# Kernel optimization log

Measured on AMD Instinct MI355X. Metric: run time of the kernel, lower is better.

The kernel has to match this reference:

```python
import jax, jax.numpy as jnp
import numpy as np

N = 100000        # nodes
E = 1600000       # edges (avg degree 16)
F_IN = 64         # num_node_features
NHID = 64         # args.nhid
NCLS = 16         # num_classes
K1 = 8            # Chebyshev order of conv1


def setup_inputs() -> dict:
    key = jax.random.key(0)
    k0, k1, k2, k3 = jax.random.split(key, 4)
    x = jax.random.normal(k0, (N, F_IN), dtype=jnp.float32)
    edge_index = jax.random.randint(k1, (2, E), 0, N, dtype=jnp.int32)
    # ChebConv params: K linear maps (no per-lin bias) + one shared bias
    W1 = jax.random.normal(k2, (K1, F_IN, NHID), dtype=jnp.float32) * (1.0 / np.sqrt(F_IN))
    b1 = jnp.zeros((NHID,), dtype=jnp.float32)
    W2 = jax.random.normal(k3, (1, NHID, NCLS), dtype=jnp.float32) * (1.0 / np.sqrt(NHID))
    b2 = jnp.zeros((NCLS,), dtype=jnp.float32)
    return {"x": x, "edge_index": edge_index, "W1": W1, "b1": b1, "W2": W2, "b2": b2}


def _cheb_norm(edge_index, num_nodes):
    # PyG ChebConv.__norm__ with normalization='sym', lambda_max=2.0, unit edge weights:
    # remove self loops; L_hat = 2L/lambda_max - I = -D^{-1/2} A D^{-1/2}, diag = 0.
    row, col = edge_index[0], edge_index[1]
    nonself = (row != col).astype(jnp.float32)
    deg = jax.ops.segment_sum(nonself, row, num_segments=num_nodes)
    dinv = jnp.where(deg > 0, jax.lax.rsqrt(jnp.maximum(deg, 1.0)), 0.0)
    norm = -dinv[row] * dinv[col] * nonself
    return row, col, norm


def reference(x, edge_index, W1, b1, W2, b2):
    row, col, norm = _cheb_norm(edge_index, N)

    def prop(h):  # L_hat @ h via gather + scatter-add, [N,F]
        return jax.ops.segment_sum(h[col] * norm[:, None], row, num_segments=N)

    # conv1: ChebConv K=8 recursion  Tx_k = 2*L_hat*Tx_{k-1} - Tx_{k-2}
    tx_prev = x
    out = x @ W1[0]
    tx = prop(x)
    out = out + tx @ W1[1]
    for k in range(2, K1):
        tx_new = 2.0 * prop(tx) - tx_prev
        out = out + tx_new @ W1[k]
        tx_prev, tx = tx, tx_new
    h = jax.nn.relu(out + b1)
    # dropout: identity (eval mode)
    # conv2: ChebConv K=1 -> just Tx_0 = h
    logits = h @ W2[0] + b2
    return jax.nn.softmax(logits, axis=1)
```

## Files before the change

### kernel.cpp

```cpp
#include <hip/hip_runtime.h>
#include <hip/hip_fp16.h>

#define N_NODES 100000
#define N_EDGES 1600000
#define F 64
#define NCLS 16
#define K1 8
#define BSH 9
#define NBK 196
#define BROWS 512
#define BKCAP 9216
#define EPB 4096
#define COLBITS 17

using f16x8 = __attribute__((ext_vector_type(8))) _Float16;
using f32x4 = __attribute__((ext_vector_type(4))) float;

__global__ __launch_bounds__(256) void k_bucketA(const int* __restrict__ ei,
                                                 int* __restrict__ gcur,
                                                 unsigned* __restrict__ bk) {
    __shared__ int cnt[4][256];
    __shared__ int wbase[4][256];
    int tid = threadIdx.x;
    int w = tid >> 6;
    for (int i = tid; i < 1024; i += 256) ((int*)cnt)[i] = 0;
    __syncthreads();
    unsigned pe[16];
    int packed[16];
    int e0 = blockIdx.x * EPB;
#pragma unroll
    for (int u = 0; u < 16; u++) {
        int e = e0 + u * 256 + tid;
        packed[u] = -1;
        if (e < N_EDGES) {
            int r = ei[e], c = ei[N_EDGES + e];
            if (r != c) {
                int b = r >> BSH;
                pe[u] = ((unsigned)(r & (BROWS - 1)) << COLBITS) | (unsigned)c;
                int rank = atomicAdd(&cnt[w][b], 1);
                packed[u] = (rank << 8) | b;
            }
        }
    }
    __syncthreads();
    {
        int c0 = cnt[0][tid], c1 = cnt[1][tid], c2 = cnt[2][tid], c3 = cnt[3][tid];
        int tot = c0 + c1 + c2 + c3;
        int g = tot ? atomicAdd(&gcur[tid], tot) : 0;
        wbase[0][tid] = g;
        wbase[1][tid] = g + c0;
        wbase[2][tid] = g + c0 + c1;
        wbase[3][tid] = g + c0 + c1 + c2;
    }
    __syncthreads();
#pragma unroll
    for (int u = 0; u < 16; u++) {
        if (packed[u] >= 0) {
            int b = packed[u] & 255;
            int rank = packed[u] >> 8;
            bk[(size_t)b * BKCAP + wbase[w][b] + rank] = pe[u];
        }
    }
}

__global__ __launch_bounds__(256) void k_csrB(const unsigned* __restrict__ bk,
                                              const int* __restrict__ gcur,
                                              int* __restrict__ deg,
                                              float* __restrict__ dinv,
                                              int* __restrict__ rowptr,
                                              int* __restrict__ csr_col) {
    __shared__ int hist[BROWS];
    __shared__ int cur[BROWS];
    __shared__ int sd[256];
    __shared__ int sorted[BKCAP];
    int b = blockIdx.x;
    int tid = threadIdx.x;
    for (int i = tid; i < BROWS; i += 256) { hist[i] = 0; cur[i] = 0; }
    __syncthreads();
    int cnt = gcur[b];
    const unsigned* src = bk + (size_t)b * BKCAP;
    for (int i = tid; i < cnt; i += 256)
        atomicAdd(&hist[src[i] >> COLBITS], 1);
    __syncthreads();
    int v0 = hist[2 * tid], v1 = hist[2 * tid + 1];
    int s = v0 + v1;
    sd[tid] = s;
    __syncthreads();
    for (int d = 1; d < 256; d <<= 1) {
        int t = (tid >= d) ? sd[tid - d] : 0;
        __syncthreads();
        sd[tid] += t;
        __syncthreads();
    }
    int excl = sd[tid] - s;
    int rbase = b << BSH;
    int cbase = b * BKCAP;
    int gr0 = rbase + 2 * tid;
    int gr1 = gr0 + 1;
    if (gr0 < N_NODES) {
        deg[gr0] = v0;
        dinv[gr0] = v0 > 0 ? rsqrtf((float)v0) : 0.f;
        rowptr[gr0] = cbase + excl;
    }
    if (gr1 < N_NODES) {
        deg[gr1] = v1;
        dinv[gr1] = v1 > 0 ? rsqrtf((float)v1) : 0.f;
        rowptr[gr1] = cbase + excl + v0;
    }
    __syncthreads();
    hist[2 * tid] = excl;
    hist[2 * tid + 1] = excl + v0;
    __syncthreads();
    for (int i = tid; i < cnt; i += 256) {
        unsigned e = src[i];
        int rl = e >> COLBITS;
        int pos = hist[rl] + atomicAdd(&cur[rl], 1);
        sorted[pos] = (int)(e & ((1u << COLBITS) - 1));
    }
    __syncthreads();
    for (int i = tid; i < cnt; i += 256)
        csr_col[cbase + i] = sorted[i];
}

__global__ void k_cvt(const float* __restrict__ x, __half* __restrict__ t0) {
    int i = blockIdx.x * blockDim.x + threadIdx.x;
    int base = i * 4;
    if (base >= N_NODES * F) return;
    float4 v = *(const float4*)&x[base];
    __half2 a = __floats2half2_rn(v.x, v.y);
    __half2 b = __floats2half2_rn(v.z, v.w);
    *(__half2*)&t0[base] = a;
    *(__half2*)&t0[base + 2] = b;
}

__global__ void k_prepW(const float* __restrict__ W1, __half* __restrict__ Wf) {
    int t = blockIdx.x * blockDim.x + threadIdx.x;
    if (t >= K1 * 2 * 4 * 64) return;
    int lane = t & 63;
    int cb = (t >> 6) & 3;
    int fg = (t >> 8) & 1;
    int kidx = t >> 9;
    int col = cb * 16 + (lane & 15);
    int kbase = fg * 32 + (lane >> 4) * 8;
    f16x8 v;
#pragma unroll
    for (int j = 0; j < 8; j++)
        v[j] = (_Float16)W1[kidx * 4096 + (kbase + j) * 64 + col];
    *(f16x8*)(Wf + (size_t)t * 8) = v;
}

__global__ __launch_bounds__(256) void k_prop(const int* __restrict__ rowptr,
                                              const int* __restrict__ deg,
                                              const int* __restrict__ csr_col,
                                              const float* __restrict__ dinv,
                                              const __half* __restrict__ src,
                                              const __half* __restrict__ prev,
                                              __half* __restrict__ dst,
                                              float alpha, float beta) {
    int wpair = (int)((blockIdx.x * blockDim.x + threadIdx.x) >> 6);
    int lane = threadIdx.x & 63;
    int nA = wpair * 2;
    if (nA >= N_NODES) return;
    int h = lane >> 5;
    int hl = lane & 31;
    int s3 = (lane >> 3) & 3;
    int fb = (lane & 7) * 8;
    int node = nA + h;
    bool valid = node < N_NODES;
    int cb  = valid ? rowptr[node] : 0;
    int end = valid ? cb + deg[node] : 0;
    float dn = valid ? dinv[node] : 0.f;

    float acc[8] = {};

    while (true) {
        int n_own = end - cb;
        if (n_own > 32) n_own = 32;
        if (n_own < 0) n_own = 0;
        int n_oth = __shfl(n_own, lane ^ 32, 64);
        int nmax = n_own > n_oth ? n_own : n_oth;
        if (nmax == 0) break;
        int col = 0;
        float dv = 0.f;
        if (hl < n_own) {
            col = csr_col[cb + hl];
            dv = dinv[col];
        }
        for (int j = 0; j < nmax; j += 16) {
            int cc[4];
            float ww[4];
#pragma unroll
            for (int g = 0; g < 4; g++) {
                int sl = (h << 5) | (j + g * 4 + s3);
                cc[g] = __shfl(col, sl, 64);
                ww[g] = __shfl(dv, sl, 64);
            }
            uint4 raw[4];
#pragma unroll
            for (int g = 0; g < 4; g++)
                raw[g] = *(const uint4*)(src + (size_t)cc[g] * F + fb);
#pragma unroll
            for (int g = 0; g < 4; g++) {
                float2 f0 = __half22float2(*(__half2*)&raw[g].x);
                float2 f1 = __half22float2(*(__half2*)&raw[g].y);
                float2 f2 = __half22float2(*(__half2*)&raw[g].z);
                float2 f3 = __half22float2(*(__half2*)&raw[g].w);
                acc[0] = fmaf(ww[g], f0.x, acc[0]);
                acc[1] = fmaf(ww[g], f0.y, acc[1]);
                acc[2] = fmaf(ww[g], f1.x, acc[2]);
                acc[3] = fmaf(ww[g], f1.y, acc[3]);
                acc[4] = fmaf(ww[g], f2.x, acc[4]);
                acc[5] = fmaf(ww[g], f2.y, acc[5]);
                acc[6] = fmaf(ww[g], f3.x, acc[6]);
                acc[7] = fmaf(ww[g], f3.y, acc[7]);
            }
        }
        cb += n_own;
    }

#pragma unroll
    for (int i = 0; i < 8; i++) {
        acc[i] += __shfl_xor(acc[i], 8, 64);
        acc[i] += __shfl_xor(acc[i], 16, 64);
    }

    if ((lane & 24) == 0 && valid) {
        float scale = -alpha * dn;
        float r[8];
#pragma unroll
        for (int i = 0; i < 8; i++) r[i] = scale * acc[i];
        if (beta != 0.f) {
            uint4 pv = *(const uint4*)(prev + (size_t)node * F + fb);
            float2 p0 = __half22float2(*(__half2*)&pv.x);
            float2 p1 = __half22float2(*(__half2*)&pv.y);
            float2 p2 = __half22float2(*(__half2*)&pv.z);
            float2 p3 = __half22float2(*(__half2*)&pv.w);
            r[0] -= beta * p0.x; r[1] -= beta * p0.y;
            r[2] -= beta * p1.x; r[3] -= beta * p1.y;
            r[4] -= beta * p2.x; r[5] -= beta * p2.y;
            r[6] -= beta * p3.x; r[7] -= beta * p3.y;
        }
        uint4 outv;
        *(__half2*)&outv.x = __floats2half2_rn(r[0], r[1]);
        *(__half2*)&outv.y = __floats2half2_rn(r[2], r[3]);
        *(__half2*)&outv.z = __floats2half2_rn(r[4], r[5]);
        *(__half2*)&outv.w = __floats2half2_rn(r[6], r[7]);
        *(uint4*)(dst + (size_t)node * F + fb) = outv;
    }
}

__global__ __launch_bounds__(256) void k_fused_mfma(const __half* __restrict__ T,
                                                    const __half* __restrict__ Wf,
                                                    const float* __restrict__ b1,
                                                    const float* __restrict__ W2,
                                                    const float* __restrict__ b2,
                                                    float* __restrict__ y) {
    __shared__ float Ht[64][65];
    __shared__ float W2l[64 * 16];
    __shared__ float b2l[16];
    int tid = threadIdx.x;
    int lane = tid & 63;
    int w = tid >> 6;
    int ln15 = lane & 15;
    int lg = lane >> 4;
    int base = blockIdx.x * 64;

    for (int j = tid; j < 64 * 16; j += 256) W2l[j] = W2[j];
    if (tid < 16) b2l[tid] = b2[tid];

    int nd = base + (w << 4) + ln15;
    if (nd > N_NODES - 1) nd = N_NODES - 1;

    f32x4 acc0 = {0.f, 0.f, 0.f, 0.f};
    f32x4 acc1 = {0.f, 0.f, 0.f, 0.f};
    f32x4 acc2 = {0.f, 0.f, 0.f, 0.f};
    f32x4 acc3 = {0.f, 0.f, 0.f, 0.f};

    for (int s = 0; s < 16; s++) {
        int kidx = s >> 1;
        int fg = s & 1;
        f16x8 a = *(const f16x8*)(T + ((size_t)kidx * N_NODES + nd) * F + fg * 32 + lg * 8);
        const __half* wb = Wf + ((size_t)((kidx * 2 + fg) * 4) * 64 + lane) * 8;
        f16x8 b0 = *(const f16x8*)(wb);
        f16x8 b1f = *(const f16x8*)(wb + 64 * 8);
        f16x8 b2f = *(const f16x8*)(wb + 128 * 8);
        f16x8 b3f = *(const f16x8*)(wb + 192 * 8);
        acc0 = __builtin_amdgcn_mfma_f32_16x16x32_f16(a, b0, acc0, 0, 0, 0);
        acc1 = __builtin_amdgcn_mfma_f32_16x16x32_f16(a, b1f, acc1, 0, 0, 0);
        acc2 = __builtin_amdgcn_mfma_f32_16x16x32_f16(a, b2f, acc2, 0, 0, 0);
        acc3 = __builtin_amdgcn_mfma_f32_16x16x32_f16(a, b3f, acc3, 0, 0, 0);
    }

    int hrow = (w << 4) + (lg << 2);
    {
        float bb0 = b1[0 * 16 + ln15];
        float bb1 = b1[1 * 16 + ln15];
        float bb2 = b1[2 * 16 + ln15];
        float bb3 = b1[3 * 16 + ln15];
#pragma unroll
        for (int r = 0; r < 4; r++) {
            float h0 = acc0[r] + bb0;
            float h1 = acc1[r] + bb1;
            float h2 = acc2[r] + bb2;
            float h3 = acc3[r] + bb3;
            Ht[hrow + r][0 * 16 + ln15] = h0 > 0.f ? h0 : 0.f;
            Ht[hrow + r][1 * 16 + ln15] = h1 > 0.f ? h1 : 0.f;
            Ht[hrow + r][2 * 16 + ln15] = h2 > 0.f ? h2 : 0.f;
            Ht[hrow + r][3 * 16 + ln15] = h3 > 0.f ? h3 : 0.f;
        }
    }
    __syncthreads();

    int node = tid >> 2;
    int cg = tid & 3;
    int gnode = base + node;
    if (gnode >= N_NODES) return;
    float l0 = b2l[cg * 4 + 0], l1 = b2l[cg * 4 + 1], l2 = b2l[cg * 4 + 2], l3 = b2l[cg * 4 + 3];
    for (int f = 0; f < 64; f++) {
        float h = Ht[node][f];
        l0 = fmaf(h, W2l[f * 16 + cg * 4 + 0], l0);
        l1 = fmaf(h, W2l[f * 16 + cg * 4 + 1], l1);
        l2 = fmaf(h, W2l[f * 16 + cg * 4 + 2], l2);
        l3 = fmaf(h, W2l[f * 16 + cg * 4 + 3], l3);
    }
    float m = fmaxf(fmaxf(l0, l1), fmaxf(l2, l3));
    m = fmaxf(m, __shfl_xor(m, 1, 64));
    m = fmaxf(m, __shfl_xor(m, 2, 64));
    float e0 = expf(l0 - m), e1 = expf(l1 - m), e2 = expf(l2 - m), e3 = expf(l3 - m);
    float s = e0 + e1 + e2 + e3;
    s += __shfl_xor(s, 1, 64);
    s += __shfl_xor(s, 2, 64);
    float inv = 1.f / s;
    float4 o = make_float4(e0 * inv, e1 * inv, e2 * inv, e3 * inv);
    *(float4*)&y[(size_t)gnode * 16 + cg * 4] = o;
}


extern "C" void kernel_launch(void* const* d_in, const int* in_sizes, int n_in,
                              void* d_out, int out_size, void* d_ws, size_t ws_size,
                              hipStream_t stream) {
    const float* x  = (const float*)d_in[0];
    const int*   ei = (const int*)d_in[1];
    const float* W1 = (const float*)d_in[2];
    const float* b1 = (const float*)d_in[3];
    const float* W2 = (const float*)d_in[4];
    const float* b2 = (const float*)d_in[5];
    float* y = (float*)d_out;

    char* p = (char*)d_ws;
    auto alloc = [&](size_t bytes) {
        char* q = p;
        p += (bytes + 255) & ~(size_t)255;
        return q;
    };
    int*   deg     = (int*)alloc((size_t)N_NODES * 4);
    float* dinv    = (float*)alloc((size_t)N_NODES * 4);
    int*   rowptr  = (int*)alloc((size_t)N_NODES * 4);
    int*   gcur    = (int*)alloc(256 * 4);
    int*   csr_col = (int*)alloc((size_t)NBK * BKCAP * 4);
    __half* T      = (__half*)alloc((size_t)K1 * N_NODES * F * 2);
    __half* Wf     = (__half*)alloc((size_t)K1 * 2 * 4 * 64 * 8 * 2);

    unsigned* bk = (unsigned*)T;

    hipMemsetAsync(gcur, 0, 256 * 4, stream);

    k_bucketA<<<(N_EDGES + EPB - 1) / EPB, 256, 0, stream>>>(ei, gcur, bk);
    k_csrB<<<NBK, 256, 0, stream>>>(bk, gcur, deg, dinv, rowptr, csr_col);
    k_prepW<<<16, 256, 0, stream>>>(W1, Wf);

    const size_t TSZ = (size_t)N_NODES * F;
    __half* Tk[K1];
    for (int k = 0; k < K1; k++) Tk[k] = T + (size_t)k * TSZ;

    k_cvt<<<(N_NODES * F / 4 + 255) / 256, 256, 0, stream>>>(x, Tk[0]);

    int npair = (N_NODES + 1) / 2;
    int prop_blocks = (npair + 3) / 4;
    k_prop<<<prop_blocks, 256, 0, stream>>>(rowptr, deg, csr_col, dinv, Tk[0], Tk[0], Tk[1], 1.f, 0.f);
    for (int k = 2; k < K1; k++)
        k_prop<<<prop_blocks, 256, 0, stream>>>(rowptr, deg, csr_col, dinv, Tk[k - 1], Tk[k - 2], Tk[k], 2.f, 1.f);

    int gemm_blocks = (N_NODES + 63) / 64;
    k_fused_mfma<<<gemm_blocks, 256, 0, stream>>>(T, Wf, b1, W2, b2, y);
}
```

Baseline: 307.8 us.

## Fuse convert, weight prep and Chebyshev propagations into one cooperative persistent kernel

Replaces the separate cvt, prepW and seven k_prop launches with a single cooperative kernel that runs persistent grid-stride loops and uses grid.sync between the recursion steps. The aim is to remove per-launch overhead and the tail idle time between dependent propagation kernels. In exchange, occupancy is capped at the cooperative grid size, work is spread by strided wave slots, and grid-wide barriers add their own cost. If the cooperative launch fails, it falls back to the old multi-kernel path.

```diff
diff --git a/kernel.cpp b/kernel.cpp
--- a/kernel.cpp
+++ b/kernel.cpp
@@ -1,5 +1,8 @@
 #include <hip/hip_runtime.h>
 #include <hip/hip_fp16.h>
+#include <hip/hip_cooperative_groups.h>
+
+namespace cg = cooperative_groups;
 
 #define N_NODES 100000
 #define N_EDGES 1600000
@@ -122,45 +125,16 @@
         csr_col[cbase + i] = sorted[i];
 }
 
-__global__ void k_cvt(const float* __restrict__ x, __half* __restrict__ t0) {
-    int i = blockIdx.x * blockDim.x + threadIdx.x;
-    int base = i * 4;
-    if (base >= N_NODES * F) return;
-    float4 v = *(const float4*)&x[base];
-    __half2 a = __floats2half2_rn(v.x, v.y);
-    __half2 b = __floats2half2_rn(v.z, v.w);
-    *(__half2*)&t0[base] = a;
-    *(__half2*)&t0[base + 2] = b;
-}
-
-__global__ void k_prepW(const float* __restrict__ W1, __half* __restrict__ Wf) {
-    int t = blockIdx.x * blockDim.x + threadIdx.x;
-    if (t >= K1 * 2 * 4 * 64) return;
-    int lane = t & 63;
-    int cb = (t >> 6) & 3;
-    int fg = (t >> 8) & 1;
-    int kidx = t >> 9;
-    int col = cb * 16 + (lane & 15);
-    int kbase = fg * 32 + (lane >> 4) * 8;
-    f16x8 v;
-#pragma unroll
-    for (int j = 0; j < 8; j++)
-        v[j] = (_Float16)W1[kidx * 4096 + (kbase + j) * 64 + col];
-    *(f16x8*)(Wf + (size_t)t * 8) = v;
-}
-
-__global__ __launch_bounds__(256) void k_prop(const int* __restrict__ rowptr,
-                                              const int* __restrict__ deg,
-                                              const int* __restrict__ csr_col,
-                                              const float* __restrict__ dinv,
-                                              const __half* __restrict__ src,
-                                              const __half* __restrict__ prev,
-                                              __half* __restrict__ dst,
-                                              float alpha, float beta) {
-    int wpair = (int)((blockIdx.x * blockDim.x + threadIdx.x) >> 6);
-    int lane = threadIdx.x & 63;
-    int nA = wpair * 2;
-    if (nA >= N_NODES) return;
+__device__ __forceinline__ void prop_body(int wp, int lane,
+                                          const int* __restrict__ rowptr,
+                                          const int* __restrict__ deg,
+                                          const int* __restrict__ csr_col,
+                                          const float* __restrict__ dinv,
+                                          const __half* __restrict__ src,
+                                          const __half* __restrict__ prev,
+                                          __half* __restrict__ dst,
+                                          float alpha, float beta) {
+    int nA = wp * 2;
     int h = lane >> 5;
     int hl = lane & 31;
     int s3 = (lane >> 3) & 3;
@@ -246,6 +220,100 @@
         *(__half2*)&outv.z = __floats2half2_rn(r[4], r[5]);
         *(__half2*)&outv.w = __floats2half2_rn(r[6], r[7]);
         *(uint4*)(dst + (size_t)node * F + fb) = outv;
+    }
+}
+
+__global__ void k_cvt(const float* __restrict__ x, __half* __restrict__ t0) {
+    int i = blockIdx.x * blockDim.x + threadIdx.x;
+    int base = i * 4;
+    if (base >= N_NODES * F) return;
+    float4 v = *(const float4*)&x[base];
+    __half2 a = __floats2half2_rn(v.x, v.y);
+    __half2 b = __floats2half2_rn(v.z, v.w);
+    *(__half2*)&t0[base] = a;
+    *(__half2*)&t0[base + 2] = b;
+}
+
+__global__ void k_prepW(const float* __restrict__ W1, __half* __restrict__ Wf) {
+    int t = blockIdx.x * blockDim.x + threadIdx.x;
+    if (t >= K1 * 2 * 4 * 64) return;
+    int lane = t & 63;
+    int cb = (t >> 6) & 3;
+    int fg = (t >> 8) & 1;
+    int kidx = t >> 9;
+    int col = cb * 16 + (lane & 15);
+    int kbase = fg * 32 + (lane >> 4) * 8;
+    f16x8 v;
+#pragma unroll
+    for (int j = 0; j < 8; j++)
+        v[j] = (_Float16)W1[kidx * 4096 + (kbase + j) * 64 + col];
+    *(f16x8*)(Wf + (size_t)t * 8) = v;
+}
+
+__global__ __launch_bounds__(256) void k_prop(const int* __restrict__ rowptr,
+                                              const int* __restrict__ deg,
+                                              const int* __restrict__ csr_col,
+                                              const float* __restrict__ dinv,
+                                              const __half* __restrict__ src,
+                                              const __half* __restrict__ prev,
+                                              __half* __restrict__ dst,
+                                              float alpha, float beta) {
+    int wp = (int)((blockIdx.x * blockDim.x + threadIdx.x) >> 6);
+    int lane = threadIdx.x & 63;
+    if (wp * 2 >= N_NODES) return;
+    prop_body(wp, lane, rowptr, deg, csr_col, dinv, src, prev, dst, alpha, beta);
+}
+
+__global__ __launch_bounds__(256, 4) void k_mega(const float* __restrict__ x,
+                                                 const float* __restrict__ W1,
+                                                 __half* __restrict__ T,
+                                                 __half* __restrict__ Wf,
+                                                 const int* __restrict__ rowptr,
+                                                 const int* __restrict__ deg,
+                                                 const int* __restrict__ csr_col,
+                                                 const float* __restrict__ dinv) {
+    cg::grid_group grid = cg::this_grid();
+    const int gthreads = gridDim.x * blockDim.x;
+    const int gtid = blockIdx.x * blockDim.x + threadIdx.x;
+    const size_t TSZ = (size_t)N_NODES * F;
+
+    for (int i = gtid; i < N_NODES * F / 4; i += gthreads) {
+        int base = i * 4;
+        float4 v = *(const float4*)&x[base];
+        __half2 a = __floats2half2_rn(v.x, v.y);
+        __half2 b = __floats2half2_rn(v.z, v.w);
+        *(__half2*)&T[base] = a;
+        *(__half2*)&T[base + 2] = b;
+    }
+    for (int t = gtid; t < K1 * 2 * 4 * 64; t += gthreads) {
+        int lane = t & 63;
+        int cb = (t >> 6) & 3;
+        int fg = (t >> 8) & 1;
+        int kidx = t >> 9;
+        int col = cb * 16 + (lane & 15);
+        int kbase = fg * 32 + (lane >> 4) * 8;
+        f16x8 v;
+#pragma unroll
+        for (int j = 0; j < 8; j++)
+            v[j] = (_Float16)W1[kidx * 4096 + (kbase + j) * 64 + col];
+        *(f16x8*)(Wf + (size_t)t * 8) = v;
+    }
+    grid.sync();
+
+    const int lane = threadIdx.x & 63;
+    const int npair = (N_NODES + 1) / 2;
+    const int nwaves = gthreads >> 6;
+    const int wslot = gtid >> 6;
+
+    for (int k = 1; k < K1; k++) {
+        const __half* src = T + (size_t)(k - 1) * TSZ;
+        const __half* prev = T + (size_t)(k >= 2 ? k - 2 : 0) * TSZ;
+        __half* dst = T + (size_t)k * TSZ;
+        const float alpha = (k == 1) ? 1.f : 2.f;
+        const float beta = (k == 1) ? 0.f : 1.f;
+        for (int wp = wslot; wp < npair; wp += nwaves)
+            prop_body(wp, lane, rowptr, deg, csr_col, dinv, src, prev, dst, alpha, beta);
+        grid.sync();
     }
 }
 
@@ -312,16 +380,16 @@
     __syncthreads();
 
     int node = tid >> 2;
-    int cg = tid & 3;
+    int cg2 = tid & 3;
     int gnode = base + node;
     if (gnode >= N_NODES) return;
-    float l0 = b2l[cg * 4 + 0], l1 = b2l[cg * 4 + 1], l2 = b2l[cg * 4 + 2], l3 = b2l[cg * 4 + 3];
+    float l0 = b2l[cg2 * 4 + 0], l1 = b2l[cg2 * 4 + 1], l2 = b2l[cg2 * 4 + 2], l3 = b2l[cg2 * 4 + 3];
     for (int f = 0; f < 64; f++) {
         float h = Ht[node][f];
-        l0 = fmaf(h, W2l[f * 16 + cg * 4 + 0], l0);
-        l1 = fmaf(h, W2l[f * 16 + cg * 4 + 1], l1);
-        l2 = fmaf(h, W2l[f * 16 + cg * 4 + 2], l2);
-        l3 = fmaf(h, W2l[f * 16 + cg * 4 + 3], l3);
+        l0 = fmaf(h, W2l[f * 16 + cg2 * 4 + 0], l0);
+        l1 = fmaf(h, W2l[f * 16 + cg2 * 4 + 1], l1);
+        l2 = fmaf(h, W2l[f * 16 + cg2 * 4 + 2], l2);
+        l3 = fmaf(h, W2l[f * 16 + cg2 * 4 + 3], l3);
     }
     float m = fmaxf(fmaxf(l0, l1), fmaxf(l2, l3));
     m = fmaxf(m, __shfl_xor(m, 1, 64));
@@ -332,7 +400,7 @@
     s += __shfl_xor(s, 2, 64);
     float inv = 1.f / s;
     float4 o = make_float4(e0 * inv, e1 * inv, e2 * inv, e3 * inv);
-    *(float4*)&y[(size_t)gnode * 16 + cg * 4] = o;
+    *(float4*)&y[(size_t)gnode * 16 + cg2 * 4] = o;
 }
 
 
@@ -367,19 +435,50 @@
 
     k_bucketA<<<(N_EDGES + EPB - 1) / EPB, 256, 0, stream>>>(ei, gcur, bk);
     k_csrB<<<NBK, 256, 0, stream>>>(bk, gcur, deg, dinv, rowptr, csr_col);
-    k_prepW<<<16, 256, 0, stream>>>(W1, Wf);
 
     const size_t TSZ = (size_t)N_NODES * F;
-    __half* Tk[K1];
-    for (int k = 0; k < K1; k++) Tk[k] = T + (size_t)k * TSZ;
-
-    k_cvt<<<(N_NODES * F / 4 + 255) / 256, 256, 0, stream>>>(x, Tk[0]);
-
-    int npair = (N_NODES + 1) / 2;
-    int prop_blocks = (npair + 3) / 4;
-    k_prop<<<prop_blocks, 256, 0, stream>>>(rowptr, deg, csr_col, dinv, Tk[0], Tk[0], Tk[1], 1.f, 0.f);
-    for (int k = 2; k < K1; k++)
-        k_prop<<<prop_blocks, 256, 0, stream>>>(rowptr, deg, csr_col, dinv, Tk[k - 1], Tk[k - 2], Tk[k], 2.f, 1.f);
+
+    bool coop_done = false;
+    {
+        int occ = 0;
+        if (hipOccupancyMaxActiveBlocksPerMultiprocessor(
+                &occ, (const void*)k_mega, 256, 0) == hipSuccess && occ >= 1) {
+            int dev = 0;
+            hipGetDevice(&dev);
+            int num_cu = 0;
+            if (hipDeviceGetAttribute(&num_cu, hipDeviceAttributeMultiprocessorCount,
+                                      dev) != hipSuccess || num_cu <= 0)
+                num_cu = 256;
+            int blocks = occ * num_cu;
+            if (blocks > 2048) blocks = 2048;
+            const float* ax = x;
+            const float* aW1 = W1;
+            __half* aT = T;
+            __half* aWf = Wf;
+            const int* arp = rowptr;
+            const int* adeg = deg;
+            const int* acc = csr_col;
+            const float* adv = dinv;
+            void* args[] = {&ax, &aW1, &aT, &aWf, &arp, &adeg, &acc, &adv};
+            hipError_t err = hipLaunchCooperativeKernel((void*)k_mega, dim3(blocks),
+                                                        dim3(256), args, 0, stream);
+            coop_done = (err == hipSuccess);
+        }
+    }
+
+    if (!coop_done) {
+        __half* Tk[K1];
+        for (int k = 0; k < K1; k++) Tk[k] = T + (size_t)k * TSZ;
+        k_cvt<<<(N_NODES * F / 4 + 255) / 256, 256, 0, stream>>>(x, Tk[0]);
+        k_prepW<<<16, 256, 0, stream>>>(W1, Wf);
+        int npair = (N_NODES + 1) / 2;
+        int prop_blocks = (npair + 3) / 4;
+        k_prop<<<prop_blocks, 256, 0, stream>>>(rowptr, deg, csr_col, dinv,
+                                                Tk[0], Tk[0], Tk[1], 1.f, 0.f);
+        for (int k = 2; k < K1; k++)
+            k_prop<<<prop_blocks, 256, 0, stream>>>(rowptr, deg, csr_col, dinv,
+                                                    Tk[k - 1], Tk[k - 2], Tk[k], 2.f, 1.f);
+    }
 
     int gemm_blocks = (N_NODES + 63) / 64;
     k_fused_mfma<<<gemm_blocks, 256, 0, stream>>>(T, Wf, b1, W2, b2, y);
```

Measured after the change: 1.123 ms. 3.65x slower.
